# Optimization experiments

Hardware: AMD Instinct MI355X
Metric: run time of the kernel (lower is better)

Reference implementation:

```python
import jax, jax.numpy as jnp
import numpy as np

H = 256  # hidden_size
B, LQ, LK = 4, 4096, 4096


def setup_inputs() -> dict:
    key = jax.random.key(0)
    ks = jax.random.split(key, 9)
    s = 1.0 / np.sqrt(H)
    return {
        "q": jax.random.normal(ks[0], (B, LQ, H), jnp.float32),
        "k": jax.random.normal(ks[1], (B, LK, H), jnp.float32),
        "v": jax.random.normal(ks[2], (B, LK, H), jnp.float32),
        "Wq": jax.random.uniform(ks[3], (H, H), jnp.float32, -s, s),
        "bq": jax.random.uniform(ks[4], (H,), jnp.float32, -s, s),
        "Wk": jax.random.uniform(ks[5], (H, H), jnp.float32, -s, s),
        "bk": jax.random.uniform(ks[6], (H,), jnp.float32, -s, s),
        "Wv": jax.random.uniform(ks[7], (H, H), jnp.float32, -s, s),
        "bv": jax.random.uniform(ks[8], (H,), jnp.float32, -s, s),
    }


def reference(q, k, v, Wq, bq, Wk, bk, Wv, bv):
    # Linear projections (torch Linear: x @ W.T + b)
    query = jnp.einsum('bsh,oh->bso', q, Wq) + bq
    keys = jnp.einsum('bsh,oh->bso', k, Wk) + bk
    values = jnp.einsum('bsh,oh->bso', v, Wv) + bv
    scores = jnp.einsum('bqh,bkh->bqk', query, keys) / jnp.sqrt(jnp.float32(H))
    weights = jax.nn.softmax(scores, axis=-1)
    context = jnp.einsum('bqk,bkh->bqh', weights, values)
    return context
```

## Files before the change

kernel.cpp:

```cpp
#include <hip/hip_runtime.h>
#include <hip/hip_bf16.h>
#include <stdint.h>

#define HD   256
#define SEQ  4096
#define NB   4
#define NTOK (NB * SEQ)
#define NEL  ((size_t)NTOK * HD)

typedef __hip_bfloat16 bf16;
typedef short    bf16x8  __attribute__((ext_vector_type(8)));
typedef float    f32x16  __attribute__((ext_vector_type(16)));
typedef float    f32x4_t __attribute__((ext_vector_type(4)));
typedef uint32_t u32x2_t __attribute__((ext_vector_type(2)));

__device__ __forceinline__ uint32_t pk2bf(float a, float b) {
  uint32_t ua = __builtin_bit_cast(uint32_t, a);
  uint32_t ub = __builtin_bit_cast(uint32_t, b);
  return ((ua + 0x8000u) >> 16) | ((ub + 0x8000u) & 0xFFFF0000u);
}
__device__ __forceinline__ uint16_t f2bf(float a) {
  uint32_t u = __builtin_bit_cast(uint32_t, a);
  return (uint16_t)((u + 0x8000u) >> 16);
}

__global__ __launch_bounds__(256, 2) void proj_kernel(
    const float* __restrict__ X, const float* __restrict__ W,
    const float* __restrict__ bias, bf16* __restrict__ out, float scale) {
  __shared__ bf16 xl[64][264];
  const int tid = (int)threadIdx.x;
  const int w = tid >> 6, l = tid & 63;
  const int m = l & 31, h = l >> 5;
  const int m0 = (int)blockIdx.x * 64;

#pragma unroll
  for (int j = 0; j < 16; ++j) {
    int e = j * 256 + tid;
    int row = e >> 6, c4 = e & 63;
    f32x4_t v = *(const f32x4_t*)(X + (size_t)(m0 + row) * HD + c4 * 4);
    u32x2_t pk; pk.x = pk2bf(v.x, v.y); pk.y = pk2bf(v.z, v.w);
    *(u32x2_t*)(&xl[row][c4 * 4]) = pk;
  }
  __syncthreads();

  f32x16 acc00 = {}, acc01 = {}, acc10 = {}, acc11 = {};

#pragma unroll
  for (int kh = 0; kh < 2; ++kh) {
    bf16x8 bfr[2][8];
#pragma unroll
    for (int nt2 = 0; nt2 < 2; ++nt2)
#pragma unroll
      for (int ks = 0; ks < 8; ++ks) {
        const float* wp = W + (size_t)(w * 64 + nt2 * 32 + m) * HD + (kh * 8 + ks) * 16 + h * 8;
        f32x4_t w0 = *(const f32x4_t*)wp;
        f32x4_t w1 = *(const f32x4_t*)(wp + 4);
        union { uint32_t u[4]; bf16x8 v; } cv;
        cv.u[0] = pk2bf(w0.x, w0.y); cv.u[1] = pk2bf(w0.z, w0.w);
        cv.u[2] = pk2bf(w1.x, w1.y); cv.u[3] = pk2bf(w1.z, w1.w);
        bfr[nt2][ks] = cv.v;
      }
#pragma unroll
    for (int ks = 0; ks < 8; ++ks) {
      int kbyte = (kh * 8 + ks) * 32 + h * 16;
      bf16x8 a0 = *(const bf16x8*)((const char*)&xl[m][0] + kbyte);
      bf16x8 a1 = *(const bf16x8*)((const char*)&xl[32 + m][0] + kbyte);
      acc00 = __builtin_amdgcn_mfma_f32_32x32x16_bf16(a0, bfr[0][ks], acc00, 0, 0, 0);
      acc01 = __builtin_amdgcn_mfma_f32_32x32x16_bf16(a0, bfr[1][ks], acc01, 0, 0, 0);
      acc10 = __builtin_amdgcn_mfma_f32_32x32x16_bf16(a1, bfr[0][ks], acc10, 0, 0, 0);
      acc11 = __builtin_amdgcn_mfma_f32_32x32x16_bf16(a1, bfr[1][ks], acc11, 0, 0, 0);
    }
  }
  __syncthreads();

  float bv0 = bias[w * 64 + m];
  float bv1 = bias[w * 64 + 32 + m];
#pragma unroll
  for (int r = 0; r < 16; ++r) {
    int row = (r & 3) + ((r >> 2) << 3) + 4 * h;
    xl[row][w * 64 + m]           = __builtin_bit_cast(bf16, f2bf((acc00[r] + bv0) * scale));
    xl[row][w * 64 + 32 + m]      = __builtin_bit_cast(bf16, f2bf((acc01[r] + bv1) * scale));
    xl[32 + row][w * 64 + m]      = __builtin_bit_cast(bf16, f2bf((acc10[r] + bv0) * scale));
    xl[32 + row][w * 64 + 32 + m] = __builtin_bit_cast(bf16, f2bf((acc11[r] + bv1) * scale));
  }
  __syncthreads();
#pragma unroll
  for (int j = 0; j < 8; ++j) {
    int unit = j * 256 + tid;
    int row = unit >> 5, uc = unit & 31;
    f32x4_t vv = *(const f32x4_t*)((const char*)&xl[row][0] + uc * 16);
    *(f32x4_t*)(out + (size_t)(m0 + row) * HD + uc * 8) = vv;
  }
}

__global__ __launch_bounds__(256, 2) void transpose_kernel(
    const bf16* __restrict__ Vp, bf16* __restrict__ Vt) {
  __shared__ bf16 tl[64][70];
  const int tid = (int)threadIdx.x;
  const int m0 = (int)blockIdx.x * 64, n0 = (int)blockIdx.y * 64;
  const int batch = m0 >> 12, s0 = m0 & (SEQ - 1);
#pragma unroll
  for (int j = 0; j < 4; ++j) {
    int unit = j * 256 + tid;
    int row = unit >> 4, qc = unit & 15;
    u32x2_t v = *(const u32x2_t*)(Vp + (size_t)(m0 + row) * HD + n0 + qc * 4);
    uint32_t* dst = (uint32_t*)&tl[row][qc * 4];
    dst[0] = v.x; dst[1] = v.y;
  }
  __syncthreads();
#pragma unroll
  for (int j = 0; j < 4; ++j) {
    int unit = j * 256 + tid;
    int orow = unit >> 4, oc = unit & 15;
    uint32_t w0 = (uint32_t)__builtin_bit_cast(uint16_t, tl[oc * 4 + 0][orow]) |
                  ((uint32_t)__builtin_bit_cast(uint16_t, tl[oc * 4 + 1][orow]) << 16);
    uint32_t w1 = (uint32_t)__builtin_bit_cast(uint16_t, tl[oc * 4 + 2][orow]) |
                  ((uint32_t)__builtin_bit_cast(uint16_t, tl[oc * 4 + 3][orow]) << 16);
    uint32_t* dst = (uint32_t*)(Vt + (size_t)batch * HD * SEQ + (size_t)(n0 + orow) * SEQ + s0 + oc * 4);
    dst[0] = w0; dst[1] = w1;
  }
}

__global__ __launch_bounds__(512, 2) void attn_kernel(
    const bf16* __restrict__ Qp, const bf16* __restrict__ Kp,
    const bf16* __restrict__ Vt, float* __restrict__ Op,
    float* __restrict__ Lp, int kvlen) {
  __shared__ __align__(128) char smem[131072];
  char* Kl = smem;
  char* Vl = smem + 65536;

  const int tid = (int)threadIdx.x;
  const int w = tid >> 6, l = tid & 63;
  const int m = l & 31, h = l >> 5;
  const int g = w >> 1, eh = w & 1;
  const int qt = (int)blockIdx.x, b = (int)blockIdx.y, sp = (int)blockIdx.z;
  const int kvbase = sp * kvlen;
  const int niter = kvlen >> 6;

  const int gq = b * SEQ + qt * 128 + g * 32 + m;
  bf16x8 qf[16];
#pragma unroll
  for (int ks = 0; ks < 16; ++ks)
    qf[ks] = *(const bf16x8*)(Qp + (size_t)gq * HD + ks * 16 + h * 8);

  f32x16 oacc[8] = {};
  float Lacc = 0.f;

  auto stage = [&](int buf, int kv0) {
#pragma unroll
    for (int i = 0; i < 4; ++i) {
      int kk = i * 16 + (tid >> 5);
      int s = tid & 31;
      int x = s ^ (kk & 31);
      const bf16* src = Kp + (size_t)(b * SEQ + kv0 + kk) * HD + x * 8;
      __builtin_amdgcn_global_load_lds(
          (const __attribute__((address_space(1))) void*)src,
          (__attribute__((address_space(3))) void*)(Kl + buf * 32768 + i * 8192 + w * 1024),
          16, 0, 0);
    }
#pragma unroll
    for (int i = 0; i < 4; ++i) {
      int row = i * 32 + (tid >> 4);
      int u = tid & 15;
      int x = u ^ (row & 15);
      int d = row * 2 + (x >> 3), c = x & 7;
      const bf16* src = Vt + (size_t)b * HD * SEQ + (size_t)d * SEQ + kv0 + c * 8;
      __builtin_amdgcn_global_load_lds(
          (const __attribute__((address_space(1))) void*)src,
          (__attribute__((address_space(3))) void*)(Vl + buf * 32768 + i * 8192 + w * 1024),
          16, 0, 0);
    }
  };

  stage(0, kvbase);
  asm volatile("s_waitcnt vmcnt(0)" ::: "memory");
  __syncthreads();

  for (int t = 0; t < niter; ++t) {
    const int cur = t & 1;
    if (t + 1 < niter) stage(cur ^ 1, kvbase + (t + 1) * 64);

    f32x16 s0 = {};
    const char* kb = Kl + cur * 32768 + (eh * 32 + m) * 512;
    __builtin_amdgcn_s_setprio(1);
#pragma unroll
    for (int ks = 0; ks < 16; ++ks) {
      bf16x8 k0 = *(const bf16x8*)(kb + (((2 * ks + h) ^ m) << 4));
      s0 = __builtin_amdgcn_mfma_f32_32x32x16_bf16(k0, qf[ks], s0, 0, 0, 0);
    }
    __builtin_amdgcn_s_setprio(0);

    float p[16];
#pragma unroll
    for (int r = 0; r < 16; ++r) p[r] = __builtin_exp2f(s0[r]);
    float ls = 0.f;
#pragma unroll
    for (int r = 0; r < 16; ++r) ls += p[r];
    Lacc += ls;

    bf16x8 pf[2];
#pragma unroll
    for (int ks = 0; ks < 2; ++ks) {
      int o = ks * 8;
      uint32_t P0 = pk2bf(p[o + 0], p[o + 1]);
      uint32_t P1 = pk2bf(p[o + 2], p[o + 3]);
      uint32_t P2 = pk2bf(p[o + 4], p[o + 5]);
      uint32_t P3 = pk2bf(p[o + 6], p[o + 7]);
      asm volatile("v_permlane32_swap_b32 %0, %1" : "+v"(P0), "+v"(P2));
      asm volatile("v_permlane32_swap_b32 %0, %1" : "+v"(P1), "+v"(P3));
      union { uint32_t u[4]; bf16x8 v; } cv;
      cv.u[0] = P0; cv.u[1] = P1; cv.u[2] = P2; cv.u[3] = P3;
      pf[ks] = cv.v;
    }

    const char* vb = Vl + cur * 32768;
    __builtin_amdgcn_s_setprio(1);
#pragma unroll
    for (int dt = 0; dt < 8; ++dt) {
      int d = dt * 32 + m;
      int vrow = d >> 1;
#pragma unroll
      for (int ks = 0; ks < 2; ++ks) {
        int u = (((d & 1) << 3) | (eh * 4 + 2 * ks + h)) ^ (vrow & 15);
        bf16x8 vf = *(const bf16x8*)(vb + vrow * 256 + u * 16);
        oacc[dt] = __builtin_amdgcn_mfma_f32_32x32x16_bf16(vf, pf[ks], oacc[dt], 0, 0, 0);
      }
    }
    __builtin_amdgcn_s_setprio(0);

    asm volatile("s_waitcnt vmcnt(0)" ::: "memory");
    __syncthreads();
  }

  float Lrow = Lacc + __shfl_xor(Lacc, 32, 64);
  if (l < 32)
    Lp[(size_t)(sp * 2 + eh) * NTOK + b * SEQ + qt * 128 + g * 32 + m] = Lrow;

  if (eh == 1) {
#pragma unroll
    for (int dt = 0; dt < 8; ++dt)
#pragma unroll
      for (int rq = 0; rq < 4; ++rq) {
        f32x4_t vv;
        vv.x = oacc[dt][rq * 4 + 0]; vv.y = oacc[dt][rq * 4 + 1];
        vv.z = oacc[dt][rq * 4 + 2]; vv.w = oacc[dt][rq * 4 + 3];
        *(f32x4_t*)(smem + g * 32768 + (dt * 4 + rq) * 1024 + l * 16) = vv;
      }
  }
  __syncthreads();
  if (eh == 0) {
#pragma unroll
    for (int dt = 0; dt < 8; ++dt)
#pragma unroll
      for (int rq = 0; rq < 4; ++rq) {
        f32x4_t vv = *(const f32x4_t*)(smem + g * 32768 + (dt * 4 + rq) * 1024 + l * 16);
        oacc[dt][rq * 4 + 0] += vv.x; oacc[dt][rq * 4 + 1] += vv.y;
        oacc[dt][rq * 4 + 2] += vv.z; oacc[dt][rq * 4 + 3] += vv.w;
      }
  }
  __syncthreads();

  if (eh == 0) {
    const int q = g * 32 + m;
#pragma unroll
    for (int dt = 0; dt < 8; ++dt)
#pragma unroll
      for (int rq = 0; rq < 4; ++rq) {
        int drow = dt * 32 + rq * 8 + 4 * h;
        f32x4_t vv;
        vv.x = oacc[dt][rq * 4 + 0]; vv.y = oacc[dt][rq * 4 + 1];
        vv.z = oacc[dt][rq * 4 + 2]; vv.w = oacc[dt][rq * 4 + 3];
        int slot = (drow >> 2) ^ (q & 31);
        *(f32x4_t*)(smem + q * 1024 + slot * 16) = vv;
      }
  }
  __syncthreads();
#pragma unroll
  for (int j = 0; j < 16; ++j) {
    int unit = j * 512 + tid;
    int qq = unit >> 6, sl = unit & 63;
    f32x4_t vv = *(const f32x4_t*)(smem + qq * 1024 + ((sl ^ (qq & 31)) << 4));
    int gqq = b * SEQ + qt * 128 + qq;
    *(f32x4_t*)(Op + (size_t)sp * NEL + (size_t)gqq * HD + sl * 4) = vv;
  }
}

__global__ __launch_bounds__(256, 2) void combine_kernel(
    const float* __restrict__ Op, const float* __restrict__ Lp,
    float* __restrict__ out, int nsplit) {
  size_t qd = (size_t)blockIdx.x * 256 + threadIdx.x;
  int row = (int)(qd >> 6);
  f32x4_t v = ((const f32x4_t*)Op)[qd];
  float Ls = Lp[row] + Lp[NTOK + row];
  if (nsplit == 2) {
    f32x4_t v2 = ((const f32x4_t*)Op)[qd + (NEL >> 2)];
    v.x += v2.x; v.y += v2.y; v.z += v2.z; v.w += v2.w;
    Ls += Lp[2 * (size_t)NTOK + row] + Lp[3 * (size_t)NTOK + row];
  }
  float inv = 1.f / Ls;
  v.x *= inv; v.y *= inv; v.z *= inv; v.w *= inv;
  ((f32x4_t*)out)[qd] = v;
}

extern "C" void kernel_launch(void* const* d_in, const int* in_sizes, int n_in,
                              void* d_out, int out_size, void* d_ws, size_t ws_size,
                              hipStream_t stream) {
  (void)in_sizes; (void)n_in; (void)out_size;
  const float* q  = (const float*)d_in[0];
  const float* k  = (const float*)d_in[1];
  const float* v  = (const float*)d_in[2];
  const float* Wq = (const float*)d_in[3];
  const float* bq = (const float*)d_in[4];
  const float* Wk = (const float*)d_in[5];
  const float* bk = (const float*)d_in[6];
  const float* Wv = (const float*)d_in[7];
  const float* bv = (const float*)d_in[8];

  char* ws = (char*)d_ws;
  bf16* Qp = (bf16*)ws;
  bf16* Kp = Qp + NEL;
  bf16* Vp = Kp + NEL;
  bf16* Vt = Vp + NEL;
  float* Op = (float*)(ws + 4 * NEL * sizeof(bf16));

  size_t need2 = 4 * NEL * sizeof(bf16) + 2 * NEL * sizeof(float) + 4 * (size_t)NTOK * sizeof(float);
  int nsplit = (ws_size >= need2) ? 2 : 1;
  float* Lp = Op + (size_t)nsplit * NEL;

  const float CEXP = 0.09016844f;

  proj_kernel<<<NTOK / 64, 256, 0, stream>>>(q, Wq, bq, Qp, CEXP);
  proj_kernel<<<NTOK / 64, 256, 0, stream>>>(k, Wk, bk, Kp, 1.0f);
  proj_kernel<<<NTOK / 64, 256, 0, stream>>>(v, Wv, bv, Vp, 1.0f);
  transpose_kernel<<<dim3(NTOK / 64, HD / 64), 256, 0, stream>>>(Vp, Vt);
  attn_kernel<<<dim3(SEQ / 128, NB, nsplit), 512, 0, stream>>>(Qp, Kp, Vt, Op, Lp, SEQ / nsplit);
  combine_kernel<<<(int)((NEL / 4) / 256), 256, 0, stream>>>(Op, Lp, (float*)d_out, nsplit);
}
```

Measured before the change: 142.2 us.

## Restructure attention to 4 waves per block, 32-key tiles, up to 4 KV splits

```diff
diff --git a/kernel.cpp b/kernel.cpp
--- a/kernel.cpp
+++ b/kernel.cpp
@@ -121,23 +121,22 @@
   }
 }
 
-__global__ __launch_bounds__(512, 2) void attn_kernel(
+__global__ __launch_bounds__(256, 2) void attn_kernel(
     const bf16* __restrict__ Qp, const bf16* __restrict__ Kp,
     const bf16* __restrict__ Vt, float* __restrict__ Op,
     float* __restrict__ Lp, int kvlen) {
-  __shared__ __align__(128) char smem[131072];
+  __shared__ __align__(128) char smem[65536];
   char* Kl = smem;
-  char* Vl = smem + 65536;
+  char* Vl = smem + 32768;
 
   const int tid = (int)threadIdx.x;
   const int w = tid >> 6, l = tid & 63;
   const int m = l & 31, h = l >> 5;
-  const int g = w >> 1, eh = w & 1;
   const int qt = (int)blockIdx.x, b = (int)blockIdx.y, sp = (int)blockIdx.z;
   const int kvbase = sp * kvlen;
-  const int niter = kvlen >> 6;
-
-  const int gq = b * SEQ + qt * 128 + g * 32 + m;
+  const int niter = kvlen >> 5;
+
+  const int gq = b * SEQ + qt * 128 + w * 32 + m;
   bf16x8 qf[16];
 #pragma unroll
   for (int ks = 0; ks < 16; ++ks)
@@ -149,25 +148,23 @@
   auto stage = [&](int buf, int kv0) {
 #pragma unroll
     for (int i = 0; i < 4; ++i) {
-      int kk = i * 16 + (tid >> 5);
-      int s = tid & 31;
-      int x = s ^ (kk & 31);
-      const bf16* src = Kp + (size_t)(b * SEQ + kv0 + kk) * HD + x * 8;
+      int kk = i * 8 + w * 2 + (l >> 5);
+      int s = (l & 31) ^ (kk & 31);
+      const bf16* src = Kp + (size_t)(b * SEQ + kv0 + kk) * HD + s * 8;
       __builtin_amdgcn_global_load_lds(
           (const __attribute__((address_space(1))) void*)src,
-          (__attribute__((address_space(3))) void*)(Kl + buf * 32768 + i * 8192 + w * 1024),
+          (__attribute__((address_space(3))) void*)(Kl + buf * 16384 + i * 4096 + w * 1024),
           16, 0, 0);
     }
 #pragma unroll
     for (int i = 0; i < 4; ++i) {
-      int row = i * 32 + (tid >> 4);
-      int u = tid & 15;
-      int x = u ^ (row & 15);
-      int d = row * 2 + (x >> 3), c = x & 7;
-      const bf16* src = Vt + (size_t)b * HD * SEQ + (size_t)d * SEQ + kv0 + c * 8;
+      int r = i * 32 + w * 8 + (l >> 3);
+      int slog = (l & 7) ^ (r & 7);
+      int d = r * 2 + (slog >> 2), j = slog & 3;
+      const bf16* src = Vt + (size_t)b * HD * SEQ + (size_t)d * SEQ + kv0 + j * 8;
       __builtin_amdgcn_global_load_lds(
           (const __attribute__((address_space(1))) void*)src,
-          (__attribute__((address_space(3))) void*)(Vl + buf * 32768 + i * 8192 + w * 1024),
+          (__attribute__((address_space(3))) void*)(Vl + buf * 16384 + i * 4096 + w * 1024),
           16, 0, 0);
     }
   };
@@ -178,10 +175,10 @@
 
   for (int t = 0; t < niter; ++t) {
     const int cur = t & 1;
-    if (t + 1 < niter) stage(cur ^ 1, kvbase + (t + 1) * 64);
+    if (t + 1 < niter) stage(cur ^ 1, kvbase + (t + 1) * 32);
 
     f32x16 s0 = {};
-    const char* kb = Kl + cur * 32768 + (eh * 32 + m) * 512;
+    const char* kb = Kl + cur * 16384 + m * 512;
     __builtin_amdgcn_s_setprio(1);
 #pragma unroll
     for (int ks = 0; ks < 16; ++ks) {
@@ -202,10 +199,11 @@
 #pragma unroll
     for (int ks = 0; ks < 2; ++ks) {
       int o = ks * 8;
-      uint32_t P0 = pk2bf(p[o + 0], p[o + 1]);
-      uint32_t P1 = pk2bf(p[o + 2], p[o + 3]);
-      uint32_t P2 = pk2bf(p[o + 4], p[o + 5]);
-      uint32_t P3 = pk2bf(p[o + 6], p[o + 7]);
+      uint32_t P0, P1, P2, P3;
+      asm("v_cvt_pk_bf16_f32 %0, %1, %2" : "=v"(P0) : "v"(p[o + 0]), "v"(p[o + 1]));
+      asm("v_cvt_pk_bf16_f32 %0, %1, %2" : "=v"(P1) : "v"(p[o + 2]), "v"(p[o + 3]));
+      asm("v_cvt_pk_bf16_f32 %0, %1, %2" : "=v"(P2) : "v"(p[o + 4]), "v"(p[o + 5]));
+      asm("v_cvt_pk_bf16_f32 %0, %1, %2" : "=v"(P3) : "v"(p[o + 6]), "v"(p[o + 7]));
       asm volatile("v_permlane32_swap_b32 %0, %1" : "+v"(P0), "+v"(P2));
       asm volatile("v_permlane32_swap_b32 %0, %1" : "+v"(P1), "+v"(P3));
       union { uint32_t u[4]; bf16x8 v; } cv;
@@ -213,16 +211,16 @@
       pf[ks] = cv.v;
     }
 
-    const char* vb = Vl + cur * 32768;
+    const char* vb = Vl + cur * 16384;
     __builtin_amdgcn_s_setprio(1);
 #pragma unroll
     for (int dt = 0; dt < 8; ++dt) {
       int d = dt * 32 + m;
-      int vrow = d >> 1;
+      int r = d >> 1;
 #pragma unroll
       for (int ks = 0; ks < 2; ++ks) {
-        int u = (((d & 1) << 3) | (eh * 4 + 2 * ks + h)) ^ (vrow & 15);
-        bf16x8 vf = *(const bf16x8*)(vb + vrow * 256 + u * 16);
+        int x = (((d & 1) << 2) | (2 * ks + h)) ^ (r & 7);
+        bf16x8 vf = *(const bf16x8*)(vb + r * 128 + x * 16);
         oacc[dt] = __builtin_amdgcn_mfma_f32_32x32x16_bf16(vf, pf[ks], oacc[dt], 0, 0, 0);
       }
     }
@@ -234,54 +232,34 @@
 
   float Lrow = Lacc + __shfl_xor(Lacc, 32, 64);
   if (l < 32)
-    Lp[(size_t)(sp * 2 + eh) * NTOK + b * SEQ + qt * 128 + g * 32 + m] = Lrow;
-
-  if (eh == 1) {
-#pragma unroll
-    for (int dt = 0; dt < 8; ++dt)
-#pragma unroll
-      for (int rq = 0; rq < 4; ++rq) {
-        f32x4_t vv;
-        vv.x = oacc[dt][rq * 4 + 0]; vv.y = oacc[dt][rq * 4 + 1];
-        vv.z = oacc[dt][rq * 4 + 2]; vv.w = oacc[dt][rq * 4 + 3];
-        *(f32x4_t*)(smem + g * 32768 + (dt * 4 + rq) * 1024 + l * 16) = vv;
-      }
-  }
-  __syncthreads();
-  if (eh == 0) {
-#pragma unroll
-    for (int dt = 0; dt < 8; ++dt)
-#pragma unroll
-      for (int rq = 0; rq < 4; ++rq) {
-        f32x4_t vv = *(const f32x4_t*)(smem + g * 32768 + (dt * 4 + rq) * 1024 + l * 16);
-        oacc[dt][rq * 4 + 0] += vv.x; oacc[dt][rq * 4 + 1] += vv.y;
-        oacc[dt][rq * 4 + 2] += vv.z; oacc[dt][rq * 4 + 3] += vv.w;
-      }
-  }
-  __syncthreads();
-
-  if (eh == 0) {
-    const int q = g * 32 + m;
-#pragma unroll
-    for (int dt = 0; dt < 8; ++dt)
-#pragma unroll
-      for (int rq = 0; rq < 4; ++rq) {
-        int drow = dt * 32 + rq * 8 + 4 * h;
-        f32x4_t vv;
-        vv.x = oacc[dt][rq * 4 + 0]; vv.y = oacc[dt][rq * 4 + 1];
-        vv.z = oacc[dt][rq * 4 + 2]; vv.w = oacc[dt][rq * 4 + 3];
-        int slot = (drow >> 2) ^ (q & 31);
-        *(f32x4_t*)(smem + q * 1024 + slot * 16) = vv;
-      }
-  }
-  __syncthreads();
-#pragma unroll
-  for (int j = 0; j < 16; ++j) {
-    int unit = j * 512 + tid;
-    int qq = unit >> 6, sl = unit & 63;
-    f32x4_t vv = *(const f32x4_t*)(smem + qq * 1024 + ((sl ^ (qq & 31)) << 4));
-    int gqq = b * SEQ + qt * 128 + qq;
-    *(f32x4_t*)(Op + (size_t)sp * NEL + (size_t)gqq * HD + sl * 4) = vv;
+    Lp[(size_t)sp * NTOK + b * SEQ + qt * 128 + w * 32 + m] = Lrow;
+
+#pragma unroll
+  for (int half = 0; half < 2; ++half) {
+    __syncthreads();
+    if ((w >> 1) == half) {
+      const int ql = (w & 1) * 32 + m;
+#pragma unroll
+      for (int dt = 0; dt < 8; ++dt)
+#pragma unroll
+        for (int rq = 0; rq < 4; ++rq) {
+          int drow = dt * 32 + rq * 8 + 4 * h;
+          f32x4_t vv;
+          vv.x = oacc[dt][rq * 4 + 0]; vv.y = oacc[dt][rq * 4 + 1];
+          vv.z = oacc[dt][rq * 4 + 2]; vv.w = oacc[dt][rq * 4 + 3];
+          int slot = (drow >> 2) ^ (ql & 31);
+          *(f32x4_t*)(smem + ql * 1024 + slot * 16) = vv;
+        }
+    }
+    __syncthreads();
+#pragma unroll
+    for (int j = 0; j < 16; ++j) {
+      int unit = j * 256 + tid;
+      int qq = unit >> 6, sl = unit & 63;
+      f32x4_t vv = *(const f32x4_t*)(smem + qq * 1024 + ((sl ^ (qq & 31)) << 4));
+      int gqq = b * SEQ + qt * 128 + half * 64 + qq;
+      *(f32x4_t*)(Op + (size_t)sp * NEL + (size_t)gqq * HD + sl * 4) = vv;
+    }
   }
 }
 
@@ -291,11 +269,11 @@
   size_t qd = (size_t)blockIdx.x * 256 + threadIdx.x;
   int row = (int)(qd >> 6);
   f32x4_t v = ((const f32x4_t*)Op)[qd];
-  float Ls = Lp[row] + Lp[NTOK + row];
-  if (nsplit == 2) {
-    f32x4_t v2 = ((const f32x4_t*)Op)[qd + (NEL >> 2)];
+  float Ls = Lp[row];
+  for (int s = 1; s < nsplit; ++s) {
+    f32x4_t v2 = ((const f32x4_t*)Op)[qd + (size_t)s * (NEL >> 2)];
     v.x += v2.x; v.y += v2.y; v.z += v2.z; v.w += v2.w;
-    Ls += Lp[2 * (size_t)NTOK + row] + Lp[3 * (size_t)NTOK + row];
+    Ls += Lp[(size_t)s * NTOK + row];
   }
   float inv = 1.f / Ls;
   v.x *= inv; v.y *= inv; v.z *= inv; v.w *= inv;
@@ -323,8 +301,12 @@
   bf16* Vt = Vp + NEL;
   float* Op = (float*)(ws + 4 * NEL * sizeof(bf16));
 
-  size_t need2 = 4 * NEL * sizeof(bf16) + 2 * NEL * sizeof(float) + 4 * (size_t)NTOK * sizeof(float);
-  int nsplit = (ws_size >= need2) ? 2 : 1;
+  int nsplit = 1;
+  for (int cand = 4; cand > 1; cand >>= 1) {
+    size_t need = 4 * NEL * sizeof(bf16) + (size_t)cand * NEL * sizeof(float) +
+                  (size_t)cand * NTOK * sizeof(float);
+    if (ws_size >= need) { nsplit = cand; break; }
+  }
   float* Lp = Op + (size_t)nsplit * NEL;
 
   const float CEXP = 0.09016844f;
@@ -333,6 +315,6 @@
   proj_kernel<<<NTOK / 64, 256, 0, stream>>>(k, Wk, bk, Kp, 1.0f);
   proj_kernel<<<NTOK / 64, 256, 0, stream>>>(v, Wv, bv, Vp, 1.0f);
   transpose_kernel<<<dim3(NTOK / 64, HD / 64), 256, 0, stream>>>(Vp, Vt);
-  attn_kernel<<<dim3(SEQ / 128, NB, nsplit), 512, 0, stream>>>(Qp, Kp, Vt, Op, Lp, SEQ / nsplit);
+  attn_kernel<<<dim3(SEQ / 128, NB, nsplit), 256, 0, stream>>>(Qp, Kp, Vt, Op, Lp, SEQ / nsplit);
   combine_kernel<<<(int)((NEL / 4) / 256), 256, 0, stream>>>(Op, Lp, (float*)d_out, nsplit);
 }
```

Measured after the change: 142.4 us. Within noise of the previous version (+0.1%).
